# Kernel tuning notes

Measured on AMD Instinct MI355X. Metric: run time of the kernel, lower is better.

## Reference

```python
import jax, jax.numpy as jnp
import numpy as np

T, B, NMUL = 730, 1000, 8
NEARZERO = 1e-5
LENF = 15
A_LO, A_HI = 0.1, 1.0
B_LO, B_HI = 50.0, 500.0
C_LO, C_HI = 0.0, 1.0
D_LO, D_HI = 0.01, 0.9
RA_LO, RA_HI = 0.0, 2.9
RB_LO, RB_HI = 0.0, 6.5
S_INIT, G_INIT = 50.0, 10.0


def setup_inputs() -> dict:
    key = jax.random.key(0)
    k1, k2 = jax.random.split(key)
    # forcing: prcp in [0,10) mm/day, pet in [0,5) mm/day
    x = jax.random.uniform(k1, (T, B, 2), dtype=jnp.float32) * jnp.array([10.0, 5.0], dtype=jnp.float32)
    # NN-produced raw params in [0,1): 4*NMUL physical + 2 routing
    raw_phy_static = jax.random.uniform(k2, (B, 4 * NMUL + 2), dtype=jnp.float32)
    return {"x": x, "raw_phy_static": raw_phy_static}


def _descale(p, lo, hi):
    return p * (hi - lo) + lo


def _uh_gamma(rout_a, rout_b):
    # gamma-distribution unit hydrograph, (B,) params -> (B, LENF) kernel
    aa = jax.nn.relu(rout_a)[:, None] + 0.1      # shape parameter
    theta = jax.nn.relu(rout_b)[:, None] + 0.5   # scale parameter
    t = jnp.arange(0.5, LENF, 1.0, dtype=jnp.float32)[None, :]  # midpoints 0.5..14.5
    logw = (aa - 1.0) * jnp.log(t) - t / theta - jax.scipy.special.gammaln(aa) - aa * jnp.log(theta)
    w = jnp.exp(logw)
    return w / w.sum(1, keepdims=True)


def _uh_conv(q, UH):
    # causal per-basin convolution: y[b,t] = sum_k q[b,t-k]*UH[b,k]; q (B,T), UH (B,LENF)
    n = q.shape[1]
    conv1 = lambda qb, wb: jnp.convolve(qb, wb, mode='full')[:n]
    return jax.vmap(conv1)(q, UH)


def reference(x, raw_phy_static):
    phy = raw_phy_static[:, :4 * NMUL].reshape(B, 4, NMUL)  # (B,4,NMUL)
    a = _descale(phy[:, 0], A_LO, A_HI)
    b = _descale(phy[:, 1], B_LO, B_HI)
    c = _descale(phy[:, 2], C_LO, C_HI)
    d = _descale(phy[:, 3], D_LO, D_HI)
    rout_a = _descale(raw_phy_static[:, 4 * NMUL], RA_LO, RA_HI)  # (B,)
    rout_b = _descale(raw_phy_static[:, 4 * NMUL + 1], RB_LO, RB_HI)

    ones_mul = jnp.ones((1, 1, NMUL), dtype=x.dtype)
    P = x[:, :, 0:1] * ones_mul    # (T,B,NMUL)
    PET = x[:, :, 1:2] * ones_mul  # (T,B,NMUL)

    S0 = jnp.full((B, NMUL), S_INIT, dtype=x.dtype)
    G0 = jnp.full((B, NMUL), G_INIT, dtype=x.dtype)

    def step(carry, inp):
        S, G = carry
        p, pet = inp
        W = p + S                                   # available water
        term = (W + b) / (2.0 * a)
        Y = term - jnp.sqrt(jnp.maximum(term * term - W * b / a, NEARZERO))  # ET opportunity
        S_new = Y * jnp.exp(-pet / b)               # soil storage
        AET = Y - S_new                             # actual ET
        avail = W - Y                               # water available for runoff/recharge
        Qsurf = (1.0 - c) * avail                   # direct runoff
        G_new = (G + c * avail) / (1.0 + d)         # groundwater storage
        Qgw = d * G_new                             # baseflow
        Qsim = Qsurf + Qgw
        return (S_new, G_new), (Qsim, Qsurf, Qgw, AET, S_new, G_new, W, Y)

    (_, _), (Qsim, Qsurf, Qgw, AET, Sout, Gout, Wout, Yout) = jax.lax.scan(step, (S0, G0), (P, PET))

    UH = _uh_gamma(rout_a, rout_b)                  # (B,LENF)
    Qs = _uh_conv(Qsim.mean(-1).T, UH).T[..., None]        # routed streamflow (T,B,1)
    Qsurf_r = _uh_conv(Qsurf.mean(-1).T, UH).T[..., None]  # routed surface runoff
    Qgw_r = _uh_conv(Qgw.mean(-1).T, UH).T[..., None]      # routed groundwater flow

    out = jnp.concatenate([
        Qs, Qsurf_r, Qgw_r,
        AET.mean(-1, keepdims=True),
        Sout.mean(-1, keepdims=True),
        Gout.mean(-1, keepdims=True),
    ], axis=-1)  # (T,B,6)
    return out
```

## Files before the change

kernel.cpp:

```cpp
#include <hip/hip_runtime.h>
#include <math.h>

#define T_STEPS 730
#define NB      1000
#define LENF    15
#define NEARZ   1e-5f
#define SGW     8000
#define TT      64
#define BBLK    32
#define NPAIR   365
#define NCHK    11


template <int CTRL>
__device__ __forceinline__ float dpp_mov(float x) {
    int xi = __builtin_bit_cast(int, x);
    int r  = __builtin_amdgcn_update_dpp(0, xi, CTRL, 0xF, 0xF, true);
    return __builtin_bit_cast(float, r);
}
__device__ __forceinline__ float sum8(float v) {
    v += dpp_mov<0xB1>(v);
    v += dpp_mov<0x4E>(v);
    v += dpp_mov<0x141>(v);
    return v;
}

#define STEPA(CURV, TB, J)                                                     \
  {                                                                            \
    float pcp = (CURV).x, pet = (CURV).y;                                      \
    float W     = pcp + S;                                                     \
    float term  = fmaf(W, inv2a, pb2a);                                        \
    float disc  = fmaf(term, term, -(W * boa));                                \
    float r     = __builtin_amdgcn_sqrtf(fmaxf(disc, NEARZ));                  \
    float Y     = term - r;                                                    \
    float e     = __builtin_amdgcn_exp2f(pet * nbl);                           \
    float Sn    = Y * e;                                                       \
    float avail = W - Y;                                                       \
    float Gn    = fmaf(pc, avail, G) * i1d;                                    \
    S = Sn; G = Gn;                                                            \
    if (((J) & 1) == 0) Skeep = Sn;                                            \
    else { *ps2 = make_float2(Skeep, Sn); ps2 += SGW; }                        \
    if ((TB) + (J) == nextchk) { *gc = Gn; gc += SGW; nextchk += TT; }         \
  }

#define PREFETCH(BUF, CI)                                                      \
  _Pragma("unroll")                                                            \
  for (int j = 0; j < 8; ++j) {                                                \
      BUF[j] = xs[((CI) * 8 + j) * 8 + bl];                                    \
  }                                                                            \
  __builtin_amdgcn_sched_barrier(0);

__global__ __launch_bounds__(64, 1) void scan_state(const float* __restrict__ x,
                                                    const float* __restrict__ raw,
                                                    float2* __restrict__ sp,
                                                    float* __restrict__ gchk) {
    __shared__ float4 xs4[2944];
    const float2* xs = (const float2*)xs4;

    const int L   = threadIdx.x;
    const int gid = blockIdx.x * 64 + L;
    const int b   = gid >> 3;
    const int m   = gid & 7;
    const int bl  = L >> 3;

    {
        float4 tmp[46];
#pragma unroll
        for (int ch = 0; ch < 46; ++ch) {
            int idx = ch * 64 + L;
            int row = idx >> 2;
            row = row < T_STEPS ? row : (T_STEPS - 1);
            tmp[ch] = *(const float4*)((const char*)x + (size_t)row * (NB * 8)
                                       + (size_t)(blockIdx.x * 64)
                                       + (size_t)(idx & 3) * 16);
        }
#pragma unroll
        for (int ch = 0; ch < 46; ++ch) xs4[ch * 64 + L] = tmp[ch];
    }
    __syncthreads();

    const float* rp = raw + b * 34;
    float pa = rp[0 * 8 + m] * 0.9f + 0.1f;
    float pb = rp[1 * 8 + m] * 450.0f + 50.0f;
    float pc = rp[2 * 8 + m];
    float pd = rp[3 * 8 + m] * 0.89f + 0.01f;

    float inv2a = 1.0f / (2.0f * pa);
    float pb2a  = pb * inv2a;
    float boa   = pb / pa;
    float nbl   = -1.4426950408889634f / pb;
    float i1d   = 1.0f / (1.0f + pd);

    float S = 50.0f, G = 10.0f, Skeep = 0.0f;
    float2* ps2 = sp + gid;
    float*  gc  = gchk + gid;
    int nextchk = TT - 15;

    float2 A[8], Bb[8], Cc[8];
    PREFETCH(A, 0)
    PREFETCH(Bb, 1)

    for (int g = 0; g < 15; ++g) {
        const int c0 = 6 * g;
        const int t0 = 48 * g;
        PREFETCH(Cc, c0 + 2)
#pragma unroll
        for (int j = 0; j < 8; ++j) STEPA(A[j],  t0,      j)
        PREFETCH(A, c0 + 3)
#pragma unroll
        for (int j = 0; j < 8; ++j) STEPA(Bb[j], t0 + 8,  j)
        PREFETCH(Bb, c0 + 4)
#pragma unroll
        for (int j = 0; j < 8; ++j) STEPA(Cc[j], t0 + 16, j)
        PREFETCH(Cc, c0 + 5)
#pragma unroll
        for (int j = 0; j < 8; ++j) STEPA(A[j],  t0 + 24, j)
        PREFETCH(A, c0 + 6)
#pragma unroll
        for (int j = 0; j < 8; ++j) STEPA(Bb[j], t0 + 32, j)
        PREFETCH(Bb, c0 + 7)
#pragma unroll
        for (int j = 0; j < 8; ++j) STEPA(Cc[j], t0 + 40, j)
    }
#pragma unroll
    for (int j = 0; j < 8; ++j) STEPA(A[j], 720, j)
    STEPA(Bb[0], 728, 0)
    STEPA(Bb[1], 728, 1)
}

#define ROW(SN, XV, TTE, RE)                                                   \
  {                                                                            \
    const int tt = (TTE); const int r = (RE);                                  \
    const bool tval = (tt >= 0) && (tt < T_STEPS);                             \
    float qs = 0.f, qg = 0.f, aet = 0.f, sX = 0.f, gX = 0.f;                   \
    if (tval) {                                                                \
      float sn  = (SN);                                                        \
      float spv = (tt == 0) ? 50.0f : Sprev;                                   \
      float y   = sn * __builtin_amdgcn_exp2f((XV).y * e2s);                   \
      float avail = ((XV).x + spv) - y;                                        \
      G = fmaf(pc, avail, G) * i1d;                                            \
      qs = omc * avail; qg = pd * G; aet = y - sn; sX = sn; gX = G;            \
      Sprev = sn;                                                              \
    }                                                                          \
    qs = sum8(qs); qg = sum8(qg);                                              \
    if (m == 0) { qsh[r][lb] = qs; qgh[r][lb] = qg; }                          \
    if (r >= 14 && tval) {                                                     \
      float a_s = sum8(aet), s_s = sum8(sX), g_s = sum8(gX);                   \
      if (bval && m < 3) {                                                     \
        float v = (m == 0) ? a_s : ((m == 1) ? s_s : g_s);                     \
        out[((size_t)tt * NB + b) * 6 + 3 + m] = v * 0.125f;                   \
      }                                                                        \
    }                                                                          \
  }

#define PAIRSTEP(PH)                                                           \
  {                                                                            \
    const int pidx = g2 * 3 + (PH);                                            \
    const int tt0  = tbase - 14 + 2 * pidx;                                    \
    float2 sv  = sb[PH];                                                       \
    float2 xv0 = x0b[PH];                                                      \
    float2 xv1 = x1b[PH];                                                      \
    { int tp = tt0 + 6; tp = tp < 0 ? 0 : (tp > 728 ? 728 : tp);               \
      sb[PH]  = sp[(size_t)(tp >> 1) * SGW + lane];                            \
      x0b[PH] = xf[tp * NB + bc];                                              \
      x1b[PH] = xf[(tp + 1) * NB + bc]; }                                      \
    ROW(sv.x, xv0, tt0,     2 * pidx)                                          \
    ROW(sv.y, xv1, tt0 + 1, 2 * pidx + 1)                                      \
  }

__global__ __launch_bounds__(256) void finalize(const float* __restrict__ x,
                                                const float* __restrict__ raw,
                                                const float2* __restrict__ sp,
                                                const float* __restrict__ gchk,
                                                float* __restrict__ out) {
    __shared__ float qsh[TT + 14][BBLK + 1];
    __shared__ float qgh[TT + 14][BBLK + 1];

    const int tid   = threadIdx.x;
    const int lb    = tid >> 3;
    const int m     = tid & 7;
    const int tbase = blockIdx.x * TT;
    const int b0    = blockIdx.y * BBLK;
    const int b     = b0 + lb;
    const bool bval = b < NB;
    const int bc    = bval ? b : (NB - 1);
    const int lane  = bc * 8 + m;

    const float* rp = raw + bc * 34;
    float pbm = rp[8 + m] * 450.0f + 50.0f;
    float e2s = 1.4426950408889634f / pbm;
    float pc  = rp[16 + m];
    float omc = 1.0f - pc;
    float pd  = rp[24 + m] * 0.89f + 0.01f;
    float i1d = 1.0f / (1.0f + pd);

    const float2* __restrict__ xf = (const float2*)x;

    float G     = (blockIdx.x == 0) ? 10.0f
                  : gchk[(size_t)(blockIdx.x - 1) * SGW + lane];
    float Sprev = 50.0f;
    if (tbase > 0) Sprev = sp[(size_t)((tbase - 16) >> 1) * SGW + lane].y;

    float2 sb[3], x0b[3], x1b[3];
#pragma unroll
    for (int d = 0; d < 3; ++d) {
        int tp = tbase - 14 + 2 * d;
        tp = tp < 0 ? 0 : (tp > 728 ? 728 : tp);
        sb[d]  = sp[(size_t)(tp >> 1) * SGW + lane];
        x0b[d] = xf[tp * NB + bc];
        x1b[d] = xf[(tp + 1) * NB + bc];
    }

    for (int g2 = 0; g2 < 13; ++g2) {
        PAIRSTEP(0)
        PAIRSTEP(1)
        PAIRSTEP(2)
    }
    __syncthreads();

    const int bl2 = tid & 31;
    const int tl0 = tid >> 5;
    const int b2  = b0 + bl2;
    if (b2 >= NB) return;

    const float* rp2 = raw + b2 * 34;
    float ra = rp2[32] * 2.9f;
    float rb = rp2[33] * 6.5f;
    float aa = fmaxf(ra, 0.0f) + 0.1f;
    float th = fmaxf(rb, 0.0f) + 0.5f;
    float inv_th = 1.0f / th;
    float am1 = aa - 1.0f;
    float w[LENF];
    float sw = 0.0f;
#pragma unroll
    for (int k = 0; k < LENF; ++k) {
        float tk = (float)k + 0.5f;
        w[k] = __expf(am1 * __logf(tk) - tk * inv_th);
        sw += w[k];
    }
    float invs = 0.125f / sw;
#pragma unroll
    for (int k = 0; k < LENF; ++k) w[k] *= invs;

#pragma unroll
    for (int it = 0; it < 8; ++it) {
        int tl = tl0 + it * 8;
        int t  = tbase + tl;
        if (t < T_STEPS) {
            float ys = 0.0f, yg = 0.0f;
#pragma unroll
            for (int k = 0; k < LENF; ++k) {
                ys = fmaf(qsh[tl + 14 - k][bl2], w[k], ys);
                yg = fmaf(qgh[tl + 14 - k][bl2], w[k], yg);
            }
            float* o = out + ((size_t)t * NB + b2) * 6;
            o[0] = ys + yg;
            o[1] = ys;
            o[2] = yg;
        }
    }
}

#define STEPF(CURV)                                                            \
  {                                                                            \
    float pcp = (CURV).x, pet = (CURV).y;                                      \
    float W     = pcp + S;                                                     \
    float term  = fmaf(W, inv2a, pb2a);                                        \
    float disc  = fmaf(term, term, -(W * boa));                                \
    float r     = __builtin_amdgcn_sqrtf(fmaxf(disc, NEARZ));                  \
    float Y     = term - r;                                                    \
    float e     = __builtin_amdgcn_exp2f(pet * ninvbl2);                       \
    float Sn    = Y * e;                                                       \
    float AET   = Y - Sn;                                                      \
    float avail = W - Y;                                                       \
    float Qs    = omc * avail;                                                 \
    float Gn    = fmaf(pc, avail, G) * inv1pd;                                 \
    float Qg    = pd * Gn;                                                     \
    S = Sn; G = Gn;                                                            \
    float qs_s = sum8(Qs);                                                     \
    float qg_s = sum8(Qg);                                                     \
    float ae_s = sum8(AET);                                                    \
    float s_s  = sum8(Sn);                                                     \
    float g_s  = sum8(Gn);                                                     \
    float v = qs_s;                                                            \
    v = (m == 1) ? qg_s : v;                                                   \
    v = (m == 2) ? ae_s : v;                                                   \
    v = (m == 3) ? s_s  : v;                                                   \
    v = (m >= 4) ? g_s  : v;                                                   \
    *optr = v * 0.125f;                                                        \
    optr += incr;                                                              \
  }

__global__ __launch_bounds__(64, 1) void scan_fb(const float* __restrict__ x,
                                                 const float* __restrict__ raw,
                                                 float* __restrict__ out,
                                                 float* __restrict__ qs_ws,
                                                 float* __restrict__ qg_ws,
                                                 float* __restrict__ dummy) {
    const int L  = threadIdx.x;
    const int lb = L >> 3;
    const int m  = L & 7;
    const int b  = blockIdx.x * 8 + lb;

    const float* rp = raw + b * 34;
    float pa = rp[0 * 8 + m] * 0.9f + 0.1f;
    float pb = rp[1 * 8 + m] * 450.0f + 50.0f;
    float pc = rp[2 * 8 + m];
    float pd = rp[3 * 8 + m] * 0.89f + 0.01f;
    float inv2a   = 1.0f / (2.0f * pa);
    float pb2a    = pb * inv2a;
    float boa     = pb / pa;
    float ninvbl2 = -1.4426950408889634f / pb;
    float omc     = 1.0f - pc;
    float inv1pd  = 1.0f / (1.0f + pd);

    float* optr;
    long long incr;
    if      (m == 0) { optr = qs_ws + b;                      incr = NB;     }
    else if (m == 1) { optr = qg_ws + b;                      incr = NB;     }
    else if (m <= 4) { optr = out + (long long)b * 6 + m + 1; incr = NB * 6; }
    else             { optr = dummy + (blockIdx.x * 64 + L);  incr = 0;      }

    float S = 50.0f, G = 10.0f;
    const float2* __restrict__ xf = (const float2*)x;

    float2 A[10], B[10], C[10];
#pragma unroll
    for (int j = 0; j < 10; ++j) A[j] = xf[j * NB + b];
#pragma unroll
    for (int j = 0; j < 10; ++j) B[j] = xf[(10 + j) * NB + b];

    for (int cg = 0; cg < 24; ++cg) {
        const int c0 = 3 * cg;
#pragma unroll
        for (int j = 0; j < 10; ++j) C[j] = xf[((c0 + 2) * 10 + j) * NB + b];
        __builtin_amdgcn_sched_barrier(0);
#pragma unroll
        for (int j = 0; j < 10; ++j) STEPF(A[j]);
#pragma unroll
        for (int j = 0; j < 10; ++j) A[j] = xf[((c0 + 3) * 10 + j) * NB + b];
        __builtin_amdgcn_sched_barrier(0);
#pragma unroll
        for (int j = 0; j < 10; ++j) STEPF(B[j]);
#pragma unroll
        for (int j = 0; j < 10; ++j) {
            int t = (c0 + 4) * 10 + j;
            t = t < T_STEPS ? t : (T_STEPS - 1);
            B[j] = xf[t * NB + b];
        }
        __builtin_amdgcn_sched_barrier(0);
#pragma unroll
        for (int j = 0; j < 10; ++j) STEPF(C[j]);
    }
#pragma unroll
    for (int j = 0; j < 10; ++j) STEPF(A[j]);
}

__global__ __launch_bounds__(256) void uh_fb(const float* __restrict__ raw,
                                             float* __restrict__ uh) {
    int b = blockIdx.x * 256 + threadIdx.x;
    if (b >= NB) return;
    float ra = raw[b * 34 + 32] * 2.9f;
    float rb = raw[b * 34 + 33] * 6.5f;
    float aa = fmaxf(ra, 0.0f) + 0.1f;
    float th = fmaxf(rb, 0.0f) + 0.5f;
    float inv_th = 1.0f / th;
    float am1 = aa - 1.0f;
    float w[LENF];
    float s = 0.0f;
#pragma unroll
    for (int k = 0; k < LENF; ++k) {
        float t = (float)k + 0.5f;
        w[k] = __expf(am1 * __logf(t) - t * inv_th);
        s += w[k];
    }
    float invs = 1.0f / s;
#pragma unroll
    for (int k = 0; k < LENF; ++k) uh[k * NB + b] = w[k] * invs;
}

__global__ __launch_bounds__(256) void conv_fb(const float* __restrict__ qs_ws,
                                               const float* __restrict__ qg_ws,
                                               const float* __restrict__ uh,
                                               float* __restrict__ out) {
    int b = blockIdx.x * 256 + threadIdx.x;
    int t = blockIdx.y;
    if (b >= NB) return;
    float ys = 0.0f, yg = 0.0f;
    int kmax = t < (LENF - 1) ? t : (LENF - 1);
    for (int k = 0; k <= kmax; ++k) {
        float w = uh[k * NB + b];
        ys = fmaf(qs_ws[(t - k) * NB + b], w, ys);
        yg = fmaf(qg_ws[(t - k) * NB + b], w, yg);
    }
    float* o = out + (t * NB + b) * 6;
    o[0] = ys + yg;
    o[1] = ys;
    o[2] = yg;
}

extern "C" void kernel_launch(void* const* d_in, const int* in_sizes, int n_in,
                              void* d_out, int out_size, void* d_ws, size_t ws_size,
                              hipStream_t stream) {
    const float* x   = (const float*)d_in[0];
    const float* raw = (const float*)d_in[1];
    float* out = (float*)d_out;

    const size_t need = (size_t)NPAIR * SGW * sizeof(float2)
                      + (size_t)NCHK * SGW * sizeof(float);
    if (ws_size >= need) {
        float2* sp   = (float2*)d_ws;
        float*  gchk = (float*)(sp + (size_t)NPAIR * SGW);
        scan_state<<<dim3(SGW / 64), dim3(64),  0, stream>>>(x, raw, sp, gchk);
        finalize  <<<dim3((T_STEPS + TT - 1) / TT, (NB + BBLK - 1) / BBLK),
                     dim3(256), 0, stream>>>(x, raw, sp, gchk, out);
    } else {
        float* qs = (float*)d_ws;
        float* qg = qs + (size_t)T_STEPS * NB;
        float* uh = qg + (size_t)T_STEPS * NB;
        float* dm = uh + (size_t)LENF * NB;
        uh_fb  <<<dim3((NB + 255) / 256),          dim3(256), 0, stream>>>(raw, uh);
        scan_fb<<<dim3(NB / 8),                    dim3(64),  0, stream>>>(x, raw, out, qs, qg, dm);
        conv_fb<<<dim3((NB + 255) / 256, T_STEPS), dim3(256), 0, stream>>>(qs, qg, uh, out);
    }
}
```

Measured before the change: 125.9 us.

## Store full S,G state per step and drop groundwater recompute in finalize

The scan kernel now writes both soil and groundwater storage for every timestep as float4 pairs, and precomputes the PET decay exponentials off the serial dependency chain. This replaces the sparse groundwater checkpoints. The finalize kernel therefore reads G directly instead of re-running the serial G recurrence from a checkpoint, so its tile shrinks from 64 to 50 timesteps and its time blocks become independent of any serial chain. The cost is doubled scan-side global write traffic and larger reads in finalize.

```diff
diff --git a/kernel.cpp b/kernel.cpp
--- a/kernel.cpp
+++ b/kernel.cpp
@@ -6,54 +6,50 @@
 #define LENF    15
 #define NEARZ   1e-5f
 #define SGW     8000
-#define TT      64
+#define NPAIR   365
+#define TT      50
 #define BBLK    32
-#define NPAIR   365
-#define NCHK    11
-
-
-template <int CTRL>
-__device__ __forceinline__ float dpp_mov(float x) {
-    int xi = __builtin_bit_cast(int, x);
-    int r  = __builtin_amdgcn_update_dpp(0, xi, CTRL, 0xF, 0xF, true);
-    return __builtin_bit_cast(float, r);
-}
-__device__ __forceinline__ float sum8(float v) {
-    v += dpp_mov<0xB1>(v);
-    v += dpp_mov<0x4E>(v);
-    v += dpp_mov<0x141>(v);
-    return v;
-}
-
-#define STEPA(CURV, TB, J)                                                     \
+
+
+#define DSLD(R, CI)                                                            \
+  _Pragma("unroll")                                                            \
+  for (int j = 0; j < 8; ++j) R[j] = xs[((CI) * 8 + j) * 8 + bl];              \
+  __builtin_amdgcn_sched_barrier(0);
+
+#define CONV(V, R)                                                             \
+  _Pragma("unroll")                                                            \
+  for (int j = 0; j < 8; ++j)                                                  \
+      V[j] = make_float2(R[j].x, __builtin_amdgcn_exp2f(R[j].y * nbl));
+
+#define STEPP(V0, V1)                                                          \
   {                                                                            \
-    float pcp = (CURV).x, pet = (CURV).y;                                      \
-    float W     = pcp + S;                                                     \
-    float term  = fmaf(W, inv2a, pb2a);                                        \
-    float disc  = fmaf(term, term, -(W * boa));                                \
-    float r     = __builtin_amdgcn_sqrtf(fmaxf(disc, NEARZ));                  \
-    float Y     = term - r;                                                    \
-    float e     = __builtin_amdgcn_exp2f(pet * nbl);                           \
-    float Sn    = Y * e;                                                       \
-    float avail = W - Y;                                                       \
-    float Gn    = fmaf(pc, avail, G) * i1d;                                    \
-    S = Sn; G = Gn;                                                            \
-    if (((J) & 1) == 0) Skeep = Sn;                                            \
-    else { *ps2 = make_float2(Skeep, Sn); ps2 += SGW; }                        \
-    if ((TB) + (J) == nextchk) { *gc = Gn; gc += SGW; nextchk += TT; }         \
+    float W0  = (V0).x + S;                                                    \
+    float t0  = fmaf(W0, inv2a, pb2a);                                         \
+    float d0  = fmaf(t0, t0, -(W0 * boa));                                     \
+    float r0  = __builtin_amdgcn_sqrtf(fmaxf(d0, NEARZ));                      \
+    float Y0  = t0 - r0;                                                       \
+    float Sn0 = Y0 * (V0).y;                                                   \
+    float av0 = W0 - Y0;                                                       \
+    float Gn0 = fmaf(pc, av0, G) * i1d;                                        \
+    float W1  = (V1).x + Sn0;                                                  \
+    float t1  = fmaf(W1, inv2a, pb2a);                                         \
+    float d1  = fmaf(t1, t1, -(W1 * boa));                                     \
+    float r1  = __builtin_amdgcn_sqrtf(fmaxf(d1, NEARZ));                      \
+    float Y1  = t1 - r1;                                                       \
+    float Sn1 = Y1 * (V1).y;                                                   \
+    float av1 = W1 - Y1;                                                       \
+    G = fmaf(pc, av1, Gn0) * i1d;                                              \
+    S = Sn1;                                                                   \
+    *ps4 = make_float4(Sn0, Gn0, Sn1, G);                                      \
+    ps4 += SGW;                                                                \
   }
 
-#define PREFETCH(BUF, CI)                                                      \
-  _Pragma("unroll")                                                            \
-  for (int j = 0; j < 8; ++j) {                                                \
-      BUF[j] = xs[((CI) * 8 + j) * 8 + bl];                                    \
-  }                                                                            \
-  __builtin_amdgcn_sched_barrier(0);
+#define CONS(V) STEPP(V[0], V[1]) STEPP(V[2], V[3])                            \
+                STEPP(V[4], V[5]) STEPP(V[6], V[7])
 
 __global__ __launch_bounds__(64, 1) void scan_state(const float* __restrict__ x,
                                                     const float* __restrict__ raw,
-                                                    float2* __restrict__ sp,
-                                                    float* __restrict__ gchk) {
+                                                    float4* __restrict__ sg4) {
     __shared__ float4 xs4[2944];
     const float2* xs = (const float2*)xs4;
 
@@ -91,44 +87,41 @@
     float nbl   = -1.4426950408889634f / pb;
     float i1d   = 1.0f / (1.0f + pd);
 
-    float S = 50.0f, G = 10.0f, Skeep = 0.0f;
-    float2* ps2 = sp + gid;
-    float*  gc  = gchk + gid;
-    int nextchk = TT - 15;
-
-    float2 A[8], Bb[8], Cc[8];
-    PREFETCH(A, 0)
-    PREFETCH(Bb, 1)
+    float S = 50.0f, G = 10.0f;
+    float4* ps4 = sg4 + gid;
+
+    float2 Ra[8], Rb[8], V0[8], V1[8], V2[8];
+    DSLD(Ra, 0)
+    DSLD(Rb, 1)
+    CONV(V0, Ra)
 
     for (int g = 0; g < 15; ++g) {
         const int c0 = 6 * g;
-        const int t0 = 48 * g;
-        PREFETCH(Cc, c0 + 2)
-#pragma unroll
-        for (int j = 0; j < 8; ++j) STEPA(A[j],  t0,      j)
-        PREFETCH(A, c0 + 3)
-#pragma unroll
-        for (int j = 0; j < 8; ++j) STEPA(Bb[j], t0 + 8,  j)
-        PREFETCH(Bb, c0 + 4)
-#pragma unroll
-        for (int j = 0; j < 8; ++j) STEPA(Cc[j], t0 + 16, j)
-        PREFETCH(Cc, c0 + 5)
-#pragma unroll
-        for (int j = 0; j < 8; ++j) STEPA(A[j],  t0 + 24, j)
-        PREFETCH(A, c0 + 6)
-#pragma unroll
-        for (int j = 0; j < 8; ++j) STEPA(Bb[j], t0 + 32, j)
-        PREFETCH(Bb, c0 + 7)
-#pragma unroll
-        for (int j = 0; j < 8; ++j) STEPA(Cc[j], t0 + 40, j)
-    }
-#pragma unroll
-    for (int j = 0; j < 8; ++j) STEPA(A[j], 720, j)
-    STEPA(Bb[0], 728, 0)
-    STEPA(Bb[1], 728, 1)
-}
-
-#define ROW(SN, XV, TTE, RE)                                                   \
+        DSLD(Ra, c0 + 2)  CONV(V1, Rb)  CONS(V0)
+        DSLD(Rb, c0 + 3)  CONV(V2, Ra)  CONS(V1)
+        DSLD(Ra, c0 + 4)  CONV(V0, Rb)  CONS(V2)
+        DSLD(Rb, c0 + 5)  CONV(V1, Ra)  CONS(V0)
+        DSLD(Ra, c0 + 6)  CONV(V2, Rb)  CONS(V1)
+        DSLD(Rb, c0 + 7)  CONV(V0, Ra)  CONS(V2)
+    }
+    CONV(V1, Rb)   CONS(V0)
+    STEPP(V1[0], V1[1])
+}
+
+template <int CTRL>
+__device__ __forceinline__ float dpp_mov(float x) {
+    int xi = __builtin_bit_cast(int, x);
+    int r  = __builtin_amdgcn_update_dpp(0, xi, CTRL, 0xF, 0xF, true);
+    return __builtin_bit_cast(float, r);
+}
+__device__ __forceinline__ float sum8(float v) {
+    v += dpp_mov<0xB1>(v);
+    v += dpp_mov<0x4E>(v);
+    v += dpp_mov<0x141>(v);
+    return v;
+}
+
+#define ROW(SN, GN, XV, TTE, RE)                                               \
   {                                                                            \
     const int tt = (TTE); const int r = (RE);                                  \
     const bool tval = (tt >= 0) && (tt < T_STEPS);                             \
@@ -138,8 +131,7 @@
       float spv = (tt == 0) ? 50.0f : Sprev;                                   \
       float y   = sn * __builtin_amdgcn_exp2f((XV).y * e2s);                   \
       float avail = ((XV).x + spv) - y;                                        \
-      G = fmaf(pc, avail, G) * i1d;                                            \
-      qs = omc * avail; qg = pd * G; aet = y - sn; sX = sn; gX = G;            \
+      qs = omc * avail; qg = dm * (GN); aet = y - sn; sX = sn; gX = (GN);      \
       Sprev = sn;                                                              \
     }                                                                          \
     qs = sum8(qs); qg = sum8(qg);                                              \
@@ -153,25 +145,9 @@
     }                                                                          \
   }
 
-#define PAIRSTEP(PH)                                                           \
-  {                                                                            \
-    const int pidx = g2 * 3 + (PH);                                            \
-    const int tt0  = tbase - 14 + 2 * pidx;                                    \
-    float2 sv  = sb[PH];                                                       \
-    float2 xv0 = x0b[PH];                                                      \
-    float2 xv1 = x1b[PH];                                                      \
-    { int tp = tt0 + 6; tp = tp < 0 ? 0 : (tp > 728 ? 728 : tp);               \
-      sb[PH]  = sp[(size_t)(tp >> 1) * SGW + lane];                            \
-      x0b[PH] = xf[tp * NB + bc];                                              \
-      x1b[PH] = xf[(tp + 1) * NB + bc]; }                                      \
-    ROW(sv.x, xv0, tt0,     2 * pidx)                                          \
-    ROW(sv.y, xv1, tt0 + 1, 2 * pidx + 1)                                      \
-  }
-
 __global__ __launch_bounds__(256) void finalize(const float* __restrict__ x,
                                                 const float* __restrict__ raw,
-                                                const float2* __restrict__ sp,
-                                                const float* __restrict__ gchk,
+                                                const float4* __restrict__ sg4,
                                                 float* __restrict__ out) {
     __shared__ float qsh[TT + 14][BBLK + 1];
     __shared__ float qgh[TT + 14][BBLK + 1];
@@ -189,32 +165,47 @@
     const float* rp = raw + bc * 34;
     float pbm = rp[8 + m] * 450.0f + 50.0f;
     float e2s = 1.4426950408889634f / pbm;
-    float pc  = rp[16 + m];
-    float omc = 1.0f - pc;
-    float pd  = rp[24 + m] * 0.89f + 0.01f;
-    float i1d = 1.0f / (1.0f + pd);
+    float omc = 1.0f - rp[16 + m];
+    float dm  = rp[24 + m] * 0.89f + 0.01f;
 
     const float2* __restrict__ xf = (const float2*)x;
-
-    float G     = (blockIdx.x == 0) ? 10.0f
-                  : gchk[(size_t)(blockIdx.x - 1) * SGW + lane];
-    float Sprev = 50.0f;
-    if (tbase > 0) Sprev = sp[(size_t)((tbase - 16) >> 1) * SGW + lane].y;
-
-    float2 sb[3], x0b[3], x1b[3];
-#pragma unroll
-    for (int d = 0; d < 3; ++d) {
-        int tp = tbase - 14 + 2 * d;
-        tp = tp < 0 ? 0 : (tp > 728 ? 728 : tp);
-        sb[d]  = sp[(size_t)(tp >> 1) * SGW + lane];
-        x0b[d] = xf[tp * NB + bc];
-        x1b[d] = xf[(tp + 1) * NB + bc];
-    }
-
-    for (int g2 = 0; g2 < 13; ++g2) {
-        PAIRSTEP(0)
-        PAIRSTEP(1)
-        PAIRSTEP(2)
+    const int Pbase = (tbase - 14) >> 1;
+
+    float4 sgb[4];
+    float2 pv0[4], pv1[4];
+#pragma unroll
+    for (int d = 0; d < 4; ++d) {
+        int P = Pbase + d; P = P < 0 ? 0 : (P > NPAIR - 1 ? NPAIR - 1 : P);
+        sgb[d] = sg4[(size_t)P * SGW + lane];
+        int t0 = tbase - 14 + 2 * d;
+        int tc0 = t0 < 0 ? 0 : (t0 > T_STEPS - 1 ? T_STEPS - 1 : t0);
+        int tc1 = t0 + 1 < 0 ? 0 : (t0 + 1 > T_STEPS - 1 ? T_STEPS - 1 : t0 + 1);
+        pv0[d] = xf[tc0 * NB + bc];
+        pv1[d] = xf[tc1 * NB + bc];
+    }
+    float Sprev = (tbase > 0)
+        ? sg4[(size_t)((tbase - 16) >> 1) * SGW + lane].z
+        : 50.0f;
+
+    for (int pp = 0; pp < 32; pp += 4) {
+#pragma unroll
+        for (int d = 0; d < 4; ++d) {
+            const int p = pp + d;
+            float4 sv = sgb[d];
+            float2 x0 = pv0[d], x1 = pv1[d];
+            {
+                int Pn = Pbase + p + 4;
+                Pn = Pn < 0 ? 0 : (Pn > NPAIR - 1 ? NPAIR - 1 : Pn);
+                sgb[d] = sg4[(size_t)Pn * SGW + lane];
+                int tn = tbase - 14 + 2 * (p + 4);
+                int tc0 = tn < 0 ? 0 : (tn > T_STEPS - 1 ? T_STEPS - 1 : tn);
+                int tc1 = tn + 1 < 0 ? 0 : (tn + 1 > T_STEPS - 1 ? T_STEPS - 1 : tn + 1);
+                pv0[d] = xf[tc0 * NB + bc];
+                pv1[d] = xf[tc1 * NB + bc];
+            }
+            ROW(sv.x, sv.y, x0, tbase - 14 + 2 * p,     2 * p)
+            ROW(sv.z, sv.w, x1, tbase - 14 + 2 * p + 1, 2 * p + 1)
+        }
     }
     __syncthreads();
 
@@ -243,10 +234,10 @@
     for (int k = 0; k < LENF; ++k) w[k] *= invs;
 
 #pragma unroll
-    for (int it = 0; it < 8; ++it) {
+    for (int it = 0; it < 7; ++it) {
         int tl = tl0 + it * 8;
         int t  = tbase + tl;
-        if (t < T_STEPS) {
+        if (tl < TT && t < T_STEPS) {
             float ys = 0.0f, yg = 0.0f;
 #pragma unroll
             for (int k = 0; k < LENF; ++k) {
@@ -406,14 +397,12 @@
     const float* raw = (const float*)d_in[1];
     float* out = (float*)d_out;
 
-    const size_t need = (size_t)NPAIR * SGW * sizeof(float2)
-                      + (size_t)NCHK * SGW * sizeof(float);
+    const size_t need = (size_t)NPAIR * SGW * sizeof(float4);
     if (ws_size >= need) {
-        float2* sp   = (float2*)d_ws;
-        float*  gchk = (float*)(sp + (size_t)NPAIR * SGW);
-        scan_state<<<dim3(SGW / 64), dim3(64),  0, stream>>>(x, raw, sp, gchk);
+        float4* sg4 = (float4*)d_ws;
+        scan_state<<<dim3(SGW / 64), dim3(64),  0, stream>>>(x, raw, sg4);
         finalize  <<<dim3((T_STEPS + TT - 1) / TT, (NB + BBLK - 1) / BBLK),
-                     dim3(256), 0, stream>>>(x, raw, sp, gchk, out);
+                     dim3(256), 0, stream>>>(x, raw, sg4, out);
     } else {
         float* qs = (float*)d_ws;
         float* qg = qs + (size_t)T_STEPS * NB;
```

New measurement: 113.0 us. -10.2%, faster.
